# Optimization experiments

Measured on AMD Instinct MI355X. Metric: run time of the kernel, lower is better.

## Reference

```python
import jax, jax.numpy as jnp
import numpy as np

EPS = 1e-8
LN_EPS = 1e-5


def _norm_no_nan(x, axis=-1, keepdims=False):
    return jnp.sqrt(jnp.clip(jnp.sum(x * x, axis=axis, keepdims=keepdims), EPS))


def gvp_apply(s, v, wh, ws_w, ws_b, wv, use_acts):
    # s: [*, si], v: [*, vi, 3]; activations = (relu, sigmoid) when use_acts
    vt = jnp.swapaxes(v, -1, -2)                        # [*, 3, vi]
    vh = jnp.matmul(vt, wh.T)                           # [*, 3, h]
    vn = _norm_no_nan(vh, axis=-2)                      # [*, h]
    s_out = jnp.matmul(jnp.concatenate([s, vn], -1), ws_w.T) + ws_b
    v_out = jnp.swapaxes(jnp.matmul(vh, wv.T), -1, -2)  # [*, vo, 3]
    if use_acts:
        v_out = v_out * jax.nn.sigmoid(_norm_no_nan(v_out, axis=-1, keepdims=True))
        s_out = jax.nn.relu(s_out)
    return s_out, v_out


def tuple_layernorm(s, v, g, b):
    mu = jnp.mean(s, -1, keepdims=True)
    var = jnp.mean(jnp.square(s - mu), -1, keepdims=True)
    s = (s - mu) / jnp.sqrt(var + LN_EPS) * g + b
    vn2 = jnp.clip(jnp.sum(v * v, -1, keepdims=True), EPS)  # [N, nv, 1]
    v = v / jnp.sqrt(jnp.mean(vn2, -2, keepdims=True))
    return s, v


def gvp_conv_layer(node_s, node_v, edge_s, edge_v, edge_index,
                   msg0_wh, msg0_wsw, msg0_wsb, msg0_wv,
                   msg1_wh, msg1_wsw, msg1_wsb, msg1_wv,
                   msg2_wh, msg2_wsw, msg2_wsb, msg2_wv,
                   ln0_g, ln0_b,
                   ff0_wh, ff0_wsw, ff0_wsb, ff0_wv,
                   ff1_wh, ff1_wsw, ff1_wsb, ff1_wv,
                   ln1_g, ln1_b):
    N = node_s.shape[0]
    src, dst = edge_index[0], edge_index[1]  # PyG: x_j = x[edge_index[0]], x_i = x[edge_index[1]]
    # gather + tuple_cat((s_j, v_j), edge_attr, (s_i, v_i))
    ms = jnp.concatenate([node_s[src], edge_s, node_s[dst]], -1)   # [E, 2*ns+es]
    mv = jnp.concatenate([node_v[src], edge_v, node_v[dst]], -2)   # [E, 2*nv+ev, 3]
    # message function: 3 GVPs, last with no activations
    ms, mv = gvp_apply(ms, mv, msg0_wh, msg0_wsw, msg0_wsb, msg0_wv, True)
    ms, mv = gvp_apply(ms, mv, msg1_wh, msg1_wsw, msg1_wsb, msg1_wv, True)
    ms, mv = gvp_apply(ms, mv, msg2_wh, msg2_wsw, msg2_wsb, msg2_wv, False)
    # mean aggregation over incoming edges per target node
    cnt = jax.ops.segment_sum(jnp.ones_like(ms[:, 0]), dst, num_segments=N)
    denom = jnp.maximum(cnt, 1.0)[:, None]
    agg_s = jax.ops.segment_sum(ms, dst, num_segments=N) / denom
    agg_v = jax.ops.segment_sum(mv, dst, num_segments=N) / denom[..., None]
    # residual + LayerNorm (dropout = identity in eval)
    s, v = tuple_layernorm(node_s + agg_s, node_v + agg_v, ln0_g, ln0_b)
    # feedforward: 2 GVPs, hidden (4*ns, 2*nv), last with no activations
    fs, fv = gvp_apply(s, v, ff0_wh, ff0_wsw, ff0_wsb, ff0_wv, True)
    fs, fv = gvp_apply(fs, fv, ff1_wh, ff1_wsw, ff1_wsb, ff1_wv, False)
    return tuple_layernorm(s + fs, v + fv, ln1_g, ln1_b)


def setup_inputs() -> dict:
    key = jax.random.key(0)
    ks = iter(jax.random.split(key, 64))
    N, E = 10000, 200000
    NS, NV, ES, EV = 128, 32, 32, 1

    def _lin(out_d, in_d):
        return jax.random.normal(next(ks), (out_d, in_d), jnp.float32) / np.float32(np.sqrt(in_d))

    inp = {
        'node_s': jax.random.normal(next(ks), (N, NS), jnp.float32),
        'node_v': jax.random.normal(next(ks), (N, NV, 3), jnp.float32),
        'edge_s': jax.random.normal(next(ks), (E, ES), jnp.float32),
        'edge_v': jax.random.normal(next(ks), (E, EV, 3), jnp.float32),
        'edge_index': jax.random.randint(next(ks), (2, E), 0, N, dtype=jnp.int32),
    }
    si0, vi0 = 2 * NS + ES, 2 * NV + EV            # 288, 65
    h0 = max(vi0, NV)                              # 65
    inp['msg0_wh'] = _lin(h0, vi0)
    inp['msg0_wsw'] = _lin(NS, h0 + si0)
    inp['msg0_wsb'] = jnp.zeros((NS,), jnp.float32)
    inp['msg0_wv'] = _lin(NV, h0)
    for name in ('msg1', 'msg2'):
        inp[name + '_wh'] = _lin(NV, NV)
        inp[name + '_wsw'] = _lin(NS, NV + NS)
        inp[name + '_wsb'] = jnp.zeros((NS,), jnp.float32)
        inp[name + '_wv'] = _lin(NV, NV)
    inp['ln0_g'] = jnp.ones((NS,), jnp.float32)
    inp['ln0_b'] = jnp.zeros((NS,), jnp.float32)
    HS, HV = 4 * NS, 2 * NV                        # 512, 64
    hf0 = max(NV, HV)                              # 64
    inp['ff0_wh'] = _lin(hf0, NV)
    inp['ff0_wsw'] = _lin(HS, hf0 + NS)
    inp['ff0_wsb'] = jnp.zeros((HS,), jnp.float32)
    inp['ff0_wv'] = _lin(HV, hf0)
    hf1 = max(HV, NV)                              # 64
    inp['ff1_wh'] = _lin(hf1, HV)
    inp['ff1_wsw'] = _lin(NS, hf1 + HS)
    inp['ff1_wsb'] = jnp.zeros((NS,), jnp.float32)
    inp['ff1_wv'] = _lin(NV, hf1)
    inp['ln1_g'] = jnp.ones((NS,), jnp.float32)
    inp['ln1_b'] = jnp.zeros((NS,), jnp.float32)
    return inp


def reference(node_s, node_v, edge_s, edge_v, edge_index,
              msg0_wh, msg0_wsw, msg0_wsb, msg0_wv,
              msg1_wh, msg1_wsw, msg1_wsb, msg1_wv,
              msg2_wh, msg2_wsw, msg2_wsb, msg2_wv,
              ln0_g, ln0_b,
              ff0_wh, ff0_wsw, ff0_wsb, ff0_wv,
              ff1_wh, ff1_wsw, ff1_wsb, ff1_wv,
              ln1_g, ln1_b):
    return gvp_conv_layer(node_s, node_v, edge_s, edge_v, edge_index,
                          msg0_wh, msg0_wsw, msg0_wsb, msg0_wv,
                          msg1_wh, msg1_wsw, msg1_wsb, msg1_wv,
                          msg2_wh, msg2_wsw, msg2_wsb, msg2_wv,
                          ln0_g, ln0_b,
                          ff0_wh, ff0_wsw, ff0_wsb, ff0_wv,
                          ff1_wh, ff1_wsw, ff1_wsb, ff1_wv,
                          ln1_g, ln1_b)
```

## Files before the change

### kernel.cpp

```cpp
#include <hip/hip_runtime.h>

typedef unsigned short u16;
typedef __attribute__((ext_vector_type(8))) short bf16x8;
typedef __attribute__((ext_vector_type(4))) float f32x4;

__device__ __forceinline__ float b2f(u16 h){ return __uint_as_float(((unsigned)h)<<16); }
__device__ __forceinline__ u16 f2b(float f){
  unsigned u = __float_as_uint(f);
  unsigned r = ((u>>16)&1u) + 0x7fffu;
  return (u16)((u+r)>>16);
}
__device__ __forceinline__ short4 pack4(float4 f){
  short4 s; s.x=(short)f2b(f.x); s.y=(short)f2b(f.y); s.z=(short)f2b(f.z); s.w=(short)f2b(f.w);
  return s;
}

#define WB0   0
#define WB1   49152
#define WB2   69632
#define WBF0  90112
#define WBF1  188416
#define WB_TOTAL 262144

#define V_WH0   0
// ... 86 lines not shown
                                              float* __restrict__ cnt){
  int e = blockIdx.x*256 + threadIdx.x;
  if (e < E) atomicAdd(&cnt[ei[(size_t)E + e]], 1.f);
}

__global__ __launch_bounds__(256) void k_scan(const float* __restrict__ cnt,
                                              int* __restrict__ wpos, int N){
  __shared__ int part[256];
  const int tid = threadIdx.x;
  const int per = (N + 255)/256;
  const int base = tid*per;
  int s = 0;
  for (int i=0;i<per;++i){ int n=base+i; if (n<N) s += (int)cnt[n]; }
  part[tid] = s; __syncthreads();
  for (int st=1; st<256; st<<=1){
    int v = (tid>=st) ? part[tid-st] : 0;
    __syncthreads();
    part[tid] += v;
    __syncthreads();
  }
  int run = part[tid] - s;
  for (int i=0;i<per;++i){ int n=base+i; if (n<N){ wpos[n]=run; run += (int)cnt[n]; } }
}

__global__ __launch_bounds__(256) void k_scatter(const int* __restrict__ ei, int E,
                                                 int* __restrict__ wpos, int* __restrict__ perm){
  int e = blockIdx.x*256 + threadIdx.x;
  if (e >= E) return;
  int d = ei[(size_t)E + e];
  int pos = atomicAdd(&wpos[d], 1);
  perm[pos] = e;
}

#define VEPB 32
__global__ __launch_bounds__(256) void k_edge_v(
    const u16* __restrict__ node_vb, const float* __restrict__ edge_v,
    const int* __restrict__ ei, int E, const int* __restrict__ perm,
    const u16* __restrict__ WVb, u16* __restrict__ vnbuf,
    float* __restrict__ agg_v, int eb, int ec)
{
  __shared__ __align__(16) char UB0[96*104*2];
  __shared__ __align__(16) u16 B1[96][104];
  __shared__ int SD[VEPB][2];
  __shared__ int GE[VEPB];
  u16 (*B0)[104] = (u16(*)[104])UB0;
  float (*SCv)[33] = (float(*)[33])UB0;
  const int tid = threadIdx.x;
  const int w = tid>>6, l = tid&63;
  const int le0 = blockIdx.x*VEPB;

  if (tid < VEPB){
    int le = le0 + tid;
    int ge = (le<ec) ? perm[eb+le] : 0;
    GE[tid] = ge;
    SD[tid][0] = ei[ge];
    SD[tid][1] = ei[(size_t)E + ge];
  }
  __syncthreads();
  for (int u=tid; u<96*16; u+=256){
    int r=u>>4, g=u&15, ee=r/3, d=r-ee*3;
    int le=le0+ee;
    short4 v = {0,0,0,0};
    if (le<ec){
      int node = (g<8) ? SD[ee][0] : SD[ee][1];
      v = *(const short4*)&node_vb[(size_t)node*96 + d*32 + 4*(g&7)];
    }
    *(short4*)&B0[r][4*g] = v;
  }
  for (int u=tid; u<96*8; u+=256){
    int r=u>>3, g=u&7, ee=r/3, d=r-ee*3;
    int le=le0+ee;
    short4 v = {0,0,0,0};
    if (g==0 && le<ec) v.x = (short)f2b(edge_v[(size_t)GE[ee]*3 + d]);
    *(short4*)&B0[r][64+4*g] = v;
  }
  for (int u=tid; u<96*4; u+=256){
    int r=u>>2, g=u&3;
    *(short4*)&B1[r][80+4*g] = (short4){0,0,0,0};
  }
  __syncthreads();

  auto mm = [&](const u16 (*A)[104], int woff, int Kp, int NT, u16 (*C)[104]){
    const int nks = Kp>>5;
    for (int t=w; t<6*NT; t+=4){
      int mt = t % 6, nt = t / 6;
      f32x4 acc = {0.f,0.f,0.f,0.f};
      for (int ks=0; ks<nks; ++ks){
        bf16x8 af = *(const bf16x8*)&A[mt*16 + (l&15)][ks*32 + (l>>4)*8];
        bf16x8 bf = *(const bf16x8*)&WVb[woff + (size_t)(nt*16 + (l&15))*Kp + ks*32 + (l>>4)*8];
        acc = __builtin_amdgcn_mfma_f32_16x16x32_bf16(af, bf, acc, 0, 0, 0);
      }
      const int col = nt*16 + (l&15);
      const int r0 = mt*16 + (l>>4)*4;
      C[r0+0][col]=f2b(acc[0]); C[r0+1][col]=f2b(acc[1]);
      C[r0+2][col]=f2b(acc[2]); C[r0+3][col]=f2b(acc[3]);
    }
  };

  mm(B0, V_WH0, 96, 5, B1);
  __syncthreads();
  for (int u=tid; u<VEPB*80; u+=256){
    int ee=u/80, h=u-ee*80;
    int le=le0+ee;
    if (le<ec){
      u16 val = 0;
      if (h<65){
        float x0=b2f(B1[ee*3+0][h]), x1=b2f(B1[ee*3+1][h]), x2=b2f(B1[ee*3+2][h]);
        val = f2b(sqrtf(fmaxf(x0*x0+x1*x1+x2*x2, 1e-8f)));
      }
      vnbuf[(size_t)le*144 + h] = val;
    }
  }
  mm(B1, V_WV0, 96, 2, B0);
  __syncthreads();
  for (int u=tid; u<VEPB*32; u+=256){
    int ee=u>>5, vo=u&31;
    float x0=b2f(B0[ee*3+0][vo]), x1=b2f(B0[ee*3+1][vo]), x2=b2f(B0[ee*3+2][vo]);
    float nn=sqrtf(fmaxf(x0*x0+x1*x1+x2*x2, 1e-8f));
    float sg=1.f/(1.f+__expf(-nn));
    B0[ee*3+0][vo]=f2b(x0*sg); B0[ee*3+1][vo]=f2b(x1*sg); B0[ee*3+2][vo]=f2b(x2*sg);
  }
  __syncthreads();
  mm(B0, V_WH1, 32, 2, B1);
  __syncthreads();
  for (int u=tid; u<VEPB*32; u+=256){
    int ee=u>>5, h=u&31;
    int le=le0+ee;
    if (le<ec){
      float x0=b2f(B1[ee*3+0][h]), x1=b2f(B1[ee*3+1][h]), x2=b2f(B1[ee*3+2][h]);
      vnbuf[(size_t)le*144 + 80 + h] = f2b(sqrtf(fmaxf(x0*x0+x1*x1+x2*x2, 1e-8f)));
    }
  }
  mm(B1, V_WV1, 32, 2, B0);
  __syncthreads();
  for (int u=tid; u<VEPB*32; u+=256){
    int ee=u>>5, vo=u&31;
    float x0=b2f(B0[ee*3+0][vo]), x1=b2f(B0[ee*3+1][vo]), x2=b2f(B0[ee*3+2][vo]);
    float nn=sqrtf(fmaxf(x0*x0+x1*x1+x2*x2, 1e-8f));
    float sg=1.f/(1.f+__expf(-nn));
    B0[ee*3+0][vo]=f2b(x0*sg); B0[ee*3+1][vo]=f2b(x1*sg); B0[ee*3+2][vo]=f2b(x2*sg);
  }
  __syncthreads();
  mm(B0, V_WH2, 32, 2, B1);
  __syncthreads();
  for (int u=tid; u<VEPB*32; u+=256){
    int ee=u>>5, h=u&31;
    int le=le0+ee;
    if (le<ec){
      float x0=b2f(B1[ee*3+0][h]), x1=b2f(B1[ee*3+1][h]), x2=b2f(B1[ee*3+2][h]);
      vnbuf[(size_t)le*144 + 112 + h] = f2b(sqrtf(fmaxf(x0*x0+x1*x1+x2*x2, 1e-8f)));
    }
  }
  for (int t=w; t<12; t+=4){
    int mt = t % 6, nt = t / 6;
    f32x4 acc = {0.f,0.f,0.f,0.f};
    bf16x8 af = *(const bf16x8*)&B1[mt*16 + (l&15)][(l>>4)*8];
    bf16x8 bf = *(const bf16x8*)&WVb[V_WV2 + (size_t)(nt*16 + (l&15))*32 + (l>>4)*8];
    acc = __builtin_amdgcn_mfma_f32_16x16x32_bf16(af, bf, acc, 0, 0, 0);
    const int vo = nt*16 + (l&15);
    const int r0 = mt*16 + (l>>4)*4;
    #pragma unroll
    for (int j=0;j<4;++j){
      int r = r0 + j;
      int le = le0 + r/3;
      SCv[r][vo] = (le < ec) ? acc[j] : 0.f;
    }
  }
  __syncthreads();
  if (tid < 96){
    const int vo = tid & 31, d = tid >> 5;
    float run = 0.f; int prev = -1;
    for (int ee=0; ee<VEPB; ++ee){
      int le = le0 + ee;
      int dn = (le<ec) ? SD[ee][1] : -1;
      if (dn != prev){
        if (prev >= 0) atomicAdd(&agg_v[(size_t)prev*96 + vo*3 + d], run);
        run = 0.f; prev = dn;
      }
      run += SCv[ee*3+d][vo];
    }
    if (prev >= 0) atomicAdd(&agg_v[(size_t)prev*96 + vo*3 + d], run);
  }
}

#define SPB 32
__global__ __launch_bounds__(512) void k_edge_s(
    const u16* __restrict__ node_sb, const float* __restrict__ edge_s,
    const int* __restrict__ ei, int E, const int* __restrict__ perm,
    const u16* __restrict__ WB, const u16* __restrict__ vnbuf,
    const float* __restrict__ b0p, const float* __restrict__ b1p, const float* __restrict__ b2p,
    float* __restrict__ agg_s, int eb, int ec)
{
  __shared__ __align__(16) char UA[SPB*392*2];
  __shared__ int SD[SPB][2];
  __shared__ int GE[SPB];
  u16 (*A)[392] = (u16(*)[392])UA;
  float (*SC)[132] = (float(*)[132])UA;
  const int tid = threadIdx.x;
  const int le0 = blockIdx.x*SPB;

  if (tid < SPB){
    int le = le0 + tid;
    int ge = (le<ec) ? perm[eb+le] : 0;
    GE[tid] = ge;
    SD[tid][0] = ei[ge];
    SD[tid][1] = ei[(size_t)E + ge];
  }
  __syncthreads();
  for (int u=tid; u<SPB*98; u+=512){
    int ee = u/98, g = u - ee*98;
    int le = le0+ee;
    short4 v = {0,0,0,0};
    if (le<ec){
      if (g < 32)      v = *(const short4*)&node_sb[(size_t)SD[ee][0]*128 + 4*g];
      else if (g < 40) v = pack4(*(const float4*)&edge_s[(size_t)GE[ee]*32 + 4*(g-32)]);
      else if (g < 72) v = *(const short4*)&node_sb[(size_t)SD[ee][1]*128 + 4*(g-40)];
      else if (g < 92) v = *(const short4*)&vnbuf[(size_t)le*144 + 4*(g-72)];
    }
    *(short4*)&A[ee][4*g] = v;
  }
  __syncthreads();

  const int w = tid>>6, l = tid&63;
  const int mt = w>>2, nt = w&3;
  const int n_a = nt*32 + (l&15), n_b = n_a + 16;
  const int kq = (l>>4)*8;
  const int ma = mt*16 + (l&15);
  f32x4 ca = {0.f,0.f,0.f,0.f}, cb = {0.f,0.f,0.f,0.f};

  for (int kk=0; kk<384; kk+=32){
    bf16x8 af = *(const bf16x8*)&A[ma][kk + kq];
    bf16x8 b1 = *(const bf16x8*)&WB[WB0 + (size_t)n_a*384 + kk + kq];
    bf16x8 b2 = *(const bf16x8*)&WB[WB0 + (size_t)n_b*384 + kk + kq];
    ca = __builtin_amdgcn_mfma_f32_16x16x32_bf16(af, b1, ca, 0, 0, 0);
    cb = __builtin_amdgcn_mfma_f32_16x16x32_bf16(af, b2, cb, 0, 0, 0);
  }
  __syncthreads();
  {
    float ba = b0p[n_a], bb = b0p[n_b];
    #pragma unroll
    for (int j=0;j<4;++j){
      int r = mt*16 + (l>>4)*4 + j;
      A[r][n_a] = f2b(fmaxf(ca[j] + ba, 0.f));
      A[r][n_b] = f2b(fmaxf(cb[j] + bb, 0.f));
    }
  }
  for (int u=tid; u<SPB*8; u+=512){
    int ee=u>>3, q=u&7;
    int le=le0+ee;
    short4 v = {0,0,0,0};
    if (le<ec) v = *(const short4*)&vnbuf[(size_t)le*144 + 80 + 4*q];
    *(short4*)&A[ee][128+4*q] = v;
  }
  __syncthreads();

  ca = (f32x4){0.f,0.f,0.f,0.f}; cb = (f32x4){0.f,0.f,0.f,0.f};
  for (int kk=0; kk<160; kk+=32){
    bf16x8 af = *(const bf16x8*)&A[ma][kk + kq];
    bf16x8 b1 = *(const bf16x8*)&WB[WB1 + (size_t)n_a*160 + kk + kq];
    bf16x8 b2 = *(const bf16x8*)&WB[WB1 + (size_t)n_b*160 + kk + kq];
    ca = __builtin_amdgcn_mfma_f32_16x16x32_bf16(af, b1, ca, 0, 0, 0);
    cb = __builtin_amdgcn_mfma_f32_16x16x32_bf16(af, b2, cb, 0, 0, 0);
  }
  __syncthreads();
  {
    float ba = b1p[n_a], bb = b1p[n_b];
    #pragma unroll
    for (int j=0;j<4;++j){
      int r = mt*16 + (l>>4)*4 + j;
      A[r][n_a] = f2b(fmaxf(ca[j] + ba, 0.f));
      A[r][n_b] = f2b(fmaxf(cb[j] + bb, 0.f));
    }
  }
  for (int u=tid; u<SPB*8; u+=512){
    int ee=u>>3, q=u&7;
    int le=le0+ee;
    short4 v = {0,0,0,0};
    if (le<ec) v = *(const short4*)&vnbuf[(size_t)le*144 + 112 + 4*q];
    *(short4*)&A[ee][128+4*q] = v;
  }
  __syncthreads();

  ca = (f32x4){0.f,0.f,0.f,0.f}; cb = (f32x4){0.f,0.f,0.f,0.f};
  for (int kk=0; kk<160; kk+=32){
    bf16x8 af = *(const bf16x8*)&A[ma][kk + kq];
    bf16x8 b1 = *(const bf16x8*)&WB[WB2 + (size_t)n_a*160 + kk + kq];
    bf16x8 b2 = *(const bf16x8*)&WB[WB2 + (size_t)n_b*160 + kk + kq];
    ca = __builtin_amdgcn_mfma_f32_16x16x32_bf16(af, b1, ca, 0, 0, 0);
    cb = __builtin_amdgcn_mfma_f32_16x16x32_bf16(af, b2, cb, 0, 0, 0);
  }
  __syncthreads();
  {
    float ba = b2p[n_a], bb = b2p[n_b];
    #pragma unroll
    for (int j=0;j<4;++j){
      int r = mt*16 + (l>>4)*4 + j;
      int le = le0 + r;
      SC[r][n_a] = (le<ec) ? (ca[j] + ba) : 0.f;
      SC[r][n_b] = (le<ec) ? (cb[j] + bb) : 0.f;
    }
  }
  __syncthreads();
  if (tid < 128){
    const int c = tid;
    float run = 0.f; int prev = -1;
    for (int r=0; r<SPB; ++r){
      int le = le0 + r;
      int dn = (le<ec) ? SD[r][1] : -1;
      if (dn != prev){
        if (prev >= 0) atomicAdd(&agg_s[(size_t)prev*128 + c], run);
        run = 0.f; prev = dn;
      }
      run += SC[r][c];
    }
    if (prev >= 0) atomicAdd(&agg_s[(size_t)prev*128 + c], run);
  }
}

__global__ __launch_bounds__(256) void k_ln0(
    const float* __restrict__ node_s, const float* __restrict__ node_v,
    const float* __restrict__ agg_s, const float* __restrict__ agg_v,
    const float* __restrict__ cnt,
    const float* __restrict__ g, const float* __restrict__ b,
    float* __restrict__ s_mid, float* __restrict__ v_mid, int N)
{
  int n = blockIdx.x*256 + threadIdx.x;
  if (n>=N) return;
  const float inv = 1.f/fmaxf(cnt[n], 1.f);
  float sum=0.f, ss=0.f;
  for (int i=0;i<128;++i){
    float x = node_s[(size_t)n*128+i] + agg_s[(size_t)n*128+i]*inv;
    sum += x; ss += x*x;
  }
  const float mu = sum*(1.f/128.f);
  const float var = fmaxf(ss*(1.f/128.f) - mu*mu, 0.f);
  const float rstd = rsqrtf(var + 1e-5f);
  for (int i=0;i<128;++i){
    float x = node_s[(size_t)n*128+i] + agg_s[(size_t)n*128+i]*inv;
    s_mid[(size_t)n*128+i] = (x-mu)*rstd*g[i] + b[i];
  }
  float vs=0.f;
  for (int vo=0;vo<32;++vo){
    float y0 = node_v[(size_t)n*96+vo*3+0] + agg_v[(size_t)n*96+vo*3+0]*inv;
    float y1 = node_v[(size_t)n*96+vo*3+1] + agg_v[(size_t)n*96+vo*3+1]*inv;
    float y2 = node_v[(size_t)n*96+vo*3+2] + agg_v[(size_t)n*96+vo*3+2]*inv;
    vs += fmaxf(y0*y0+y1*y1+y2*y2, 1e-8f);
  }
  const float scale = rsqrtf(vs*(1.f/32.f));
  for (int vo=0;vo<32;++vo){
    float y0 = node_v[(size_t)n*96+vo*3+0] + agg_v[(size_t)n*96+vo*3+0]*inv;
    float y1 = node_v[(size_t)n*96+vo*3+1] + agg_v[(size_t)n*96+vo*3+1]*inv;
    float y2 = node_v[(size_t)n*96+vo*3+2] + agg_v[(size_t)n*96+vo*3+2]*inv;
    v_mid[(size_t)n*96+vo]      = y0*scale;
    v_mid[(size_t)n*96+32+vo]   = y1*scale;
    v_mid[(size_t)n*96+64+vo]   = y2*scale;
  }
}

__global__ __launch_bounds__(256) void k_node_v(
    const float* __restrict__ v_mid, const u16* __restrict__ WVb,
    u16* __restrict__ vn0f, u16* __restrict__ vn1f, float* __restrict__ fv1, int N)
{
  __shared__ __align__(16) u16 B0[96][104];
  __shared__ __align__(16) u16 B1[96][104];
  const int tid = threadIdx.x;
  const int w = tid>>6, l = tid&63;
  const int n0 = blockIdx.x*32;

  for (int u=tid; u<96*8; u+=256){
    int r=u>>3, g=u&7, nd=r/3, d=r-nd*3;
    int n=n0+nd;
    short4 v = {0,0,0,0};
    if (n<N) v = pack4(*(const float4*)&v_mid[(size_t)n*96 + d*32 + 4*g]);
    *(short4*)&B0[r][4*g] = v;
  }
  __syncthreads();

  auto mm = [&](const u16 (*A)[104], int woff, int Kp, int NT, u16 (*C)[104]){
    const int nks = Kp>>5;
    for (int t=w; t<6*NT; t+=4){
      int mt = t % 6, nt = t / 6;
      f32x4 acc = {0.f,0.f,0.f,0.f};
      for (int ks=0; ks<nks; ++ks){
        bf16x8 af = *(const bf16x8*)&A[mt*16 + (l&15)][ks*32 + (l>>4)*8];
        bf16x8 bf = *(const bf16x8*)&WVb[woff + (size_t)(nt*16 + (l&15))*Kp + ks*32 + (l>>4)*8];
        acc = __builtin_amdgcn_mfma_f32_16x16x32_bf16(af, bf, acc, 0, 0, 0);
      }
      const int col = nt*16 + (l&15);
      const int r0 = mt*16 + (l>>4)*4;
      C[r0+0][col]=f2b(acc[0]); C[r0+1][col]=f2b(acc[1]);
      C[r0+2][col]=f2b(acc[2]); C[r0+3][col]=f2b(acc[3]);
    }
  };

  mm(B0, NV_FF0H, 32, 4, B1);
  __syncthreads();
  for (int u=tid; u<32*64; u+=256){
    int nd=u>>6, h=u&63;
    int n=n0+nd;
    if (n<N){
      float x0=b2f(B1[nd*3+0][h]), x1=b2f(B1[nd*3+1][h]), x2=b2f(B1[nd*3+2][h]);
      vn0f[(size_t)n*64+h] = f2b(sqrtf(fmaxf(x0*x0+x1*x1+x2*x2, 1e-8f)));
    }
  }
  mm(B1, NV_FF0V, 64, 4, B0);
  __syncthreads();
  for (int u=tid; u<32*64; u+=256){
    int nd=u>>6, vo=u&63;
    float x0=b2f(B0[nd*3+0][vo]), x1=b2f(B0[nd*3+1][vo]), x2=b2f(B0[nd*3+2][vo]);
    float nn=sqrtf(fmaxf(x0*x0+x1*x1+x2*x2, 1e-8f));
    float sg=1.f/(1.f+__expf(-nn));
    B0[nd*3+0][vo]=f2b(x0*sg); B0[nd*3+1][vo]=f2b(x1*sg); B0[nd*3+2][vo]=f2b(x2*sg);
  }
  __syncthreads();
  mm(B0, NV_FF1H, 64, 4, B1);
  __syncthreads();
  for (int u=tid; u<32*64; u+=256){
    int nd=u>>6, h=u&63;
    int n=n0+nd;
    if (n<N){
      float x0=b2f(B1[nd*3+0][h]), x1=b2f(B1[nd*3+1][h]), x2=b2f(B1[nd*3+2][h]);
      vn1f[(size_t)n*64+h] = f2b(sqrtf(fmaxf(x0*x0+x1*x1+x2*x2, 1e-8f)));
    }
  }
  for (int t=w; t<12; t+=4){
    int mt = t % 6, nt = t / 6;
    f32x4 acc = {0.f,0.f,0.f,0.f};
// ... 110 lines not shown
      }
    }
    float z[2][3]; float vs = 0.f;
    #pragma unroll
    for (int j=0;j<2;++j){
      int vo = q + 16*j;
      #pragma unroll
      for (int d=0;d<3;++d){
        float y = live ? (v_mid[(size_t)n*96 + d*32 + vo] + fv1[(size_t)n*96 + d*32 + vo]) : 0.f;
        z[j][d] = y;
      }
      vs += fmaxf(z[j][0]*z[j][0]+z[j][1]*z[j][1]+z[j][2]*z[j][2], 1e-8f);
    }
    #pragma unroll
    for (int m=1; m<16; m<<=1) vs += __shfl_xor(vs, m);
    const float scale = rsqrtf(vs*(1.f/32.f));
    if (live){
      size_t base = (size_t)N*128 + (size_t)n*96;
      #pragma unroll
      for (int j=0;j<2;++j){
        int vo = q + 16*j;
        out[base + vo*3 + 0] = z[j][0]*scale;
        out[base + vo*3 + 1] = z[j][1]*scale;
        out[base + vo*3 + 2] = z[j][2]*scale;
      }
    }
  }
}

extern "C" void kernel_launch(void* const* d_in, const int* in_sizes, int n_in,
                              void* d_out, int out_size, void* d_ws, size_t ws_size,
                              hipStream_t stream)
{
  (void)n_in; (void)out_size;
  const int N = in_sizes[0]/128;
  const int E = in_sizes[4]/2;
  const int* ei = (const int*)d_in[4];

  size_t off = 0;
  auto alloc = [&](size_t bytes)->char*{
    size_t o = (off + 255) & ~(size_t)255;
    off = o + bytes;
    return (char*)d_ws + o;
  };
  u16*   WB      = (u16*)alloc((size_t)WB_TOTAL*2);
  u16*   WVb     = (u16*)alloc((size_t)WV_TOTAL*2);
  float* agg_s   = (float*)alloc((size_t)N*128*4);
  float* agg_v   = (float*)alloc((size_t)N*96*4);
  float* cnt     = (float*)alloc((size_t)N*4);
  size_t aggBytes = (size_t)((char*)(cnt+N) - (char*)agg_s);
  float* s_mid   = (float*)alloc((size_t)N*128*4);
  float* v_mid   = (float*)alloc((size_t)N*96*4);
  u16*   node_sb = (u16*)alloc((size_t)N*128*2);
  u16*   node_vb = (u16*)alloc((size_t)N*96*2);
  u16*   vn0f    = (u16*)alloc((size_t)N*64*2);
  u16*   vn1f    = (u16*)alloc((size_t)N*64*2);
  float* fv1     = (float*)alloc((size_t)N*96*4);
  int*   wpos    = (int*)alloc((size_t)N*4);
  int*   perm    = (int*)alloc((size_t)E*4);
  const size_t persist_end = off;

  size_t avail = (ws_size > persist_end + (1u<<20)) ? (ws_size - persist_end - (1u<<20)) : 0;
  long EC = (long)(avail / 288);
  if (EC < 8192) EC = 8192;
  if (EC > E) EC = E;
  u16* vnbuf = (u16*)alloc((size_t)EC*144*2);

  hipMemsetAsync(agg_s, 0, aggBytes, stream);
  k_wb<<<dim3((WB_TOTAL+255)/256), dim3(256), 0, stream>>>(
      (const float*)d_in[6], (const float*)d_in[10], (const float*)d_in[14],
      (const float*)d_in[20], (const float*)d_in[24], WB);
  k_wv<<<dim3((WV_TOTAL+255)/256), dim3(256), 0, stream>>>(
      (const float*)d_in[5], (const float*)d_in[8], (const float*)d_in[9],
      (const float*)d_in[12], (const float*)d_in[13], (const float*)d_in[16],
      (const float*)d_in[19], (const float*)d_in[22], (const float*)d_in[23],
      (const float*)d_in[26], WVb);
  k_prep<<<dim3((N*224+255)/256), dim3(256), 0, stream>>>(
      (const float*)d_in[0], (const float*)d_in[1], node_sb, node_vb, N);
  k_hist<<<dim3((E+255)/256), dim3(256), 0, stream>>>(ei, E, cnt);
  k_scan<<<dim3(1), dim3(256), 0, stream>>>(cnt, wpos, N);
  k_scatter<<<dim3((E+255)/256), dim3(256), 0, stream>>>(ei, E, wpos, perm);

  const int nch = (int)((E + EC - 1)/EC);
  for (int c=0; c<nch; ++c){
    const int eb = c*(int)EC;
    int ec = E - eb; if (ec > (int)EC) ec = (int)EC;
    if (ec <= 0) break;
    k_edge_v<<<dim3((ec+VEPB-1)/VEPB), dim3(256), 0, stream>>>(
        node_vb, (const float*)d_in[3], ei, E, perm, WVb, vnbuf, agg_v, eb, ec);
    k_edge_s<<<dim3((ec+SPB-1)/SPB), dim3(512), 0, stream>>>(
        node_sb, (const float*)d_in[2], ei, E, perm, WB, vnbuf,
        (const float*)d_in[7], (const float*)d_in[11], (const float*)d_in[15],
        agg_s, eb, ec);
  }

  k_ln0<<<dim3((N+255)/256), dim3(256), 0, stream>>>(
      (const float*)d_in[0], (const float*)d_in[1], agg_s, agg_v, cnt,
      (const float*)d_in[17], (const float*)d_in[18], s_mid, v_mid, N);

  k_node_v<<<dim3((N+31)/32), dim3(256), 0, stream>>>(v_mid, WVb, vn0f, vn1f, fv1, N);
  k_node_s<<<dim3((N+31)/32), dim3(512), 0, stream>>>(
      s_mid, vn0f, vn1f, v_mid, fv1, WB,
      (const float*)d_in[21], (const float*)d_in[25],
      (const float*)d_in[27], (const float*)d_in[28],
      (float*)d_out, N);
}
```

Measured before the change: 587.4 us.

## Fuse edge vector and scalar message kernels into one block-level kernel

Merges the separate edge-vector and edge-scalar kernels into a single 512-thread kernel, so the vector-norm features stay in shared memory instead of making a round trip through a global vnbuf. The chunked edge loop and its workspace sizing go away, and the whole edge set is launched at once. The vector-GVP matmuls now spread their tiles over 8 waves instead of 4, and the kernel's shared-memory footprint grows to about 50KB, which may reduce occupancy.

Measured after the change: 568.6 us. 3.2% less time.

```diff
diff --git a/kernel.cpp b/kernel.cpp
--- a/kernel.cpp
+++ b/kernel.cpp
@@ -142,51 +142,315 @@
   perm[pos] = e;
 }
 
-#define VEPB 32
-__global__ __launch_bounds__(256) void k_edge_v(
-    const u16* __restrict__ node_vb, const float* __restrict__ edge_v,
+#define EPB 32
+__global__ __launch_bounds__(512) void k_edge_fused(
+    const u16* __restrict__ node_sb, const u16* __restrict__ node_vb,
+    const float* __restrict__ edge_s, const float* __restrict__ edge_v,
     const int* __restrict__ ei, int E, const int* __restrict__ perm,
-    const u16* __restrict__ WVb, u16* __restrict__ vnbuf,
-    float* __restrict__ agg_v, int eb, int ec)
+    const u16* __restrict__ WB, const u16* __restrict__ WVb,
+    const float* __restrict__ b0p, const float* __restrict__ b1p, const float* __restrict__ b2p,
+    float* __restrict__ agg_s, float* __restrict__ agg_v)
 {
-  __shared__ __align__(16) char UB0[96*104*2];
-  __shared__ __align__(16) u16 B1[96][104];
-  __shared__ int SD[VEPB][2];
-  __shared__ int GE[VEPB];
-  u16 (*B0)[104] = (u16(*)[104])UB0;
-  float (*SCv)[33] = (float(*)[33])UB0;
+  __shared__ __align__(16) char R1[42240];
+  __shared__ __align__(16) u16 VN0[EPB][80];
+  __shared__ __align__(16) u16 VN1[EPB][32];
+  __shared__ __align__(16) u16 VN2[EPB][32];
+  __shared__ int SD[EPB][2];
+  __shared__ int GE[EPB];
+  u16 (*B0)[104]  = (u16(*)[104])R1;
+  u16 (*B1)[104]  = (u16(*)[104])(R1 + 20480);
+  float (*SCv)[33] = (float(*)[33])R1;
+  u16 (*A)[392]   = (u16(*)[392])R1;
+  float (*SC)[132] = (float(*)[132])R1;
+
   const int tid = threadIdx.x;
   const int w = tid>>6, l = tid&63;
-  const int le0 = blockIdx.x*VEPB;
-
-  if (tid < VEPB){
+  const int le0 = blockIdx.x*EPB;
+
+  if (tid < EPB){
     int le = le0 + tid;
-    int ge = (le<ec) ? perm[eb+le] : 0;
+    int ge = (le<E) ? perm[le] : 0;
     GE[tid] = ge;
     SD[tid][0] = ei[ge];
     SD[tid][1] = ei[(size_t)E + ge];
   }
   __syncthreads();
-  for (int u=tid; u<96*16; u+=256){
+  for (int u=tid; u<96*16; u+=512){
     int r=u>>4, g=u&15, ee=r/3, d=r-ee*3;
     int le=le0+ee;
     short4 v = {0,0,0,0};
-    if (le<ec){
+    if (le<E){
       int node = (g<8) ? SD[ee][0] : SD[ee][1];
       v = *(const short4*)&node_vb[(size_t)node*96 + d*32 + 4*(g&7)];
     }
     *(short4*)&B0[r][4*g] = v;
   }
-  for (int u=tid; u<96*8; u+=256){
+  for (int u=tid; u<96*8; u+=512){
     int r=u>>3, g=u&7, ee=r/3, d=r-ee*3;
     int le=le0+ee;
     short4 v = {0,0,0,0};
-    if (g==0 && le<ec) v.x = (short)f2b(edge_v[(size_t)GE[ee]*3 + d]);
+    if (g==0 && le<E) v.x = (short)f2b(edge_v[(size_t)GE[ee]*3 + d]);
     *(short4*)&B0[r][64+4*g] = v;
   }
-  for (int u=tid; u<96*4; u+=256){
+  for (int u=tid; u<96*4; u+=512){
     int r=u>>2, g=u&3;
     *(short4*)&B1[r][80+4*g] = (short4){0,0,0,0};
+  }
+  __syncthreads();
+
+  auto mm = [&](const u16 (*Ai)[104], int woff, int Kp, int NT, u16 (*C)[104]){
+    const int nks = Kp>>5;
+    for (int t=w; t<6*NT; t+=8){
+      int mt = t % 6, nt = t / 6;
+      f32x4 acc = {0.f,0.f,0.f,0.f};
+      for (int ks=0; ks<nks; ++ks){
+        bf16x8 af = *(const bf16x8*)&Ai[mt*16 + (l&15)][ks*32 + (l>>4)*8];
+        bf16x8 bf = *(const bf16x8*)&WVb[woff + (size_t)(nt*16 + (l&15))*Kp + ks*32 + (l>>4)*8];
+        acc = __builtin_amdgcn_mfma_f32_16x16x32_bf16(af, bf, acc, 0, 0, 0);
+      }
+      const int col = nt*16 + (l&15);
+      const int r0 = mt*16 + (l>>4)*4;
+      C[r0+0][col]=f2b(acc[0]); C[r0+1][col]=f2b(acc[1]);
+      C[r0+2][col]=f2b(acc[2]); C[r0+3][col]=f2b(acc[3]);
+    }
+  };
+
+  mm(B0, V_WH0, 96, 5, B1);
+  __syncthreads();
+  for (int u=tid; u<EPB*80; u+=512){
+    int ee=u/80, h=u-ee*80;
+    u16 val = 0;
+    if (h<65){
+      float x0=b2f(B1[ee*3+0][h]), x1=b2f(B1[ee*3+1][h]), x2=b2f(B1[ee*3+2][h]);
+      val = f2b(sqrtf(fmaxf(x0*x0+x1*x1+x2*x2, 1e-8f)));
+    }
+    VN0[ee][h] = val;
+  }
+  mm(B1, V_WV0, 96, 2, B0);
+  __syncthreads();
+  for (int u=tid; u<EPB*32; u+=512){
+    int ee=u>>5, vo=u&31;
+    float x0=b2f(B0[ee*3+0][vo]), x1=b2f(B0[ee*3+1][vo]), x2=b2f(B0[ee*3+2][vo]);
+    float nn=sqrtf(fmaxf(x0*x0+x1*x1+x2*x2, 1e-8f));
+    float sg=1.f/(1.f+__expf(-nn));
+    B0[ee*3+0][vo]=f2b(x0*sg); B0[ee*3+1][vo]=f2b(x1*sg); B0[ee*3+2][vo]=f2b(x2*sg);
+  }
+  __syncthreads();
+  mm(B0, V_WH1, 32, 2, B1);
+  __syncthreads();
+  for (int u=tid; u<EPB*32; u+=512){
+    int ee=u>>5, h=u&31;
+    float x0=b2f(B1[ee*3+0][h]), x1=b2f(B1[ee*3+1][h]), x2=b2f(B1[ee*3+2][h]);
+    VN1[ee][h] = f2b(sqrtf(fmaxf(x0*x0+x1*x1+x2*x2, 1e-8f)));
+  }
+  mm(B1, V_WV1, 32, 2, B0);
+  __syncthreads();
+  for (int u=tid; u<EPB*32; u+=512){
+    int ee=u>>5, vo=u&31;
+    float x0=b2f(B0[ee*3+0][vo]), x1=b2f(B0[ee*3+1][vo]), x2=b2f(B0[ee*3+2][vo]);
+    float nn=sqrtf(fmaxf(x0*x0+x1*x1+x2*x2, 1e-8f));
+    float sg=1.f/(1.f+__expf(-nn));
+    B0[ee*3+0][vo]=f2b(x0*sg); B0[ee*3+1][vo]=f2b(x1*sg); B0[ee*3+2][vo]=f2b(x2*sg);
+  }
+  __syncthreads();
+  mm(B0, V_WH2, 32, 2, B1);
+  __syncthreads();
+  for (int u=tid; u<EPB*32; u+=512){
+    int ee=u>>5, h=u&31;
+    float x0=b2f(B1[ee*3+0][h]), x1=b2f(B1[ee*3+1][h]), x2=b2f(B1[ee*3+2][h]);
+    VN2[ee][h] = f2b(sqrtf(fmaxf(x0*x0+x1*x1+x2*x2, 1e-8f)));
+  }
+  for (int t=w; t<12; t+=8){
+    int mt = t % 6, nt = t / 6;
+    f32x4 acc = {0.f,0.f,0.f,0.f};
+    bf16x8 af = *(const bf16x8*)&B1[mt*16 + (l&15)][(l>>4)*8];
+    bf16x8 bf = *(const bf16x8*)&WVb[V_WV2 + (size_t)(nt*16 + (l&15))*32 + (l>>4)*8];
+    acc = __builtin_amdgcn_mfma_f32_16x16x32_bf16(af, bf, acc, 0, 0, 0);
+    const int vo = nt*16 + (l&15);
+    const int r0 = mt*16 + (l>>4)*4;
+    #pragma unroll
+    for (int j=0;j<4;++j){
+      int r = r0 + j;
+      int le = le0 + r/3;
+      SCv[r][vo] = (le < E) ? acc[j] : 0.f;
+    }
+  }
+  __syncthreads();
+  if (tid < 96){
+    const int vo = tid & 31, d = tid >> 5;
+    float run = 0.f; int prev = -1;
+    for (int ee=0; ee<EPB; ++ee){
+      int le = le0 + ee;
+      int dn = (le<E) ? SD[ee][1] : -1;
+      if (dn != prev){
+        if (prev >= 0) atomicAdd(&agg_v[(size_t)prev*96 + vo*3 + d], run);
+        run = 0.f; prev = dn;
+      }
+      run += SCv[ee*3+d][vo];
+    }
+    if (prev >= 0) atomicAdd(&agg_v[(size_t)prev*96 + vo*3 + d], run);
+  }
+  __syncthreads();
+
+  for (int u=tid; u<EPB*98; u+=512){
+    int ee = u/98, g = u - ee*98;
+    int le = le0+ee;
+    short4 v = {0,0,0,0};
+    if (le<E){
+      if (g < 32)      v = *(const short4*)&node_sb[(size_t)SD[ee][0]*128 + 4*g];
+      else if (g < 40) v = pack4(*(const float4*)&edge_s[(size_t)GE[ee]*32 + 4*(g-32)]);
+      else if (g < 72) v = *(const short4*)&node_sb[(size_t)SD[ee][1]*128 + 4*(g-40)];
+      else if (g < 92) v = *(const short4*)&VN0[ee][4*(g-72)];
+    }
+    *(short4*)&A[ee][4*g] = v;
+  }
+  __syncthreads();
+
+  const int mt = w>>2, nt = w&3;
+  const int n_a = nt*32 + (l&15), n_b = n_a + 16;
+  const int kq = (l>>4)*8;
+  const int ma = mt*16 + (l&15);
+  f32x4 ca = {0.f,0.f,0.f,0.f}, cb = {0.f,0.f,0.f,0.f};
+
+  for (int kk=0; kk<384; kk+=32){
+    bf16x8 af = *(const bf16x8*)&A[ma][kk + kq];
+    bf16x8 b1 = *(const bf16x8*)&WB[WB0 + (size_t)n_a*384 + kk + kq];
+    bf16x8 b2 = *(const bf16x8*)&WB[WB0 + (size_t)n_b*384 + kk + kq];
+    ca = __builtin_amdgcn_mfma_f32_16x16x32_bf16(af, b1, ca, 0, 0, 0);
+    cb = __builtin_amdgcn_mfma_f32_16x16x32_bf16(af, b2, cb, 0, 0, 0);
+  }
+  __syncthreads();
+  {
+    float ba = b0p[n_a], bb = b0p[n_b];
+    #pragma unroll
+    for (int j=0;j<4;++j){
+      int r = mt*16 + (l>>4)*4 + j;
+      A[r][n_a] = f2b(fmaxf(ca[j] + ba, 0.f));
+      A[r][n_b] = f2b(fmaxf(cb[j] + bb, 0.f));
+    }
+  }
+  for (int u=tid; u<EPB*8; u+=512){
+    int ee=u>>3, q=u&7;
+    *(short4*)&A[ee][128+4*q] = *(const short4*)&VN1[ee][4*q];
+  }
+  __syncthreads();
+
+  ca = (f32x4){0.f,0.f,0.f,0.f}; cb = (f32x4){0.f,0.f,0.f,0.f};
+  for (int kk=0; kk<160; kk+=32){
+    bf16x8 af = *(const bf16x8*)&A[ma][kk + kq];
+    bf16x8 b1 = *(const bf16x8*)&WB[WB1 + (size_t)n_a*160 + kk + kq];
+    bf16x8 b2 = *(const bf16x8*)&WB[WB1 + (size_t)n_b*160 + kk + kq];
+    ca = __builtin_amdgcn_mfma_f32_16x16x32_bf16(af, b1, ca, 0, 0, 0);
+    cb = __builtin_amdgcn_mfma_f32_16x16x32_bf16(af, b2, cb, 0, 0, 0);
+  }
+  __syncthreads();
+  {
+    float ba = b1p[n_a], bb = b1p[n_b];
+    #pragma unroll
+    for (int j=0;j<4;++j){
+      int r = mt*16 + (l>>4)*4 + j;
+      A[r][n_a] = f2b(fmaxf(ca[j] + ba, 0.f));
+      A[r][n_b] = f2b(fmaxf(cb[j] + bb, 0.f));
+    }
+  }
+  for (int u=tid; u<EPB*8; u+=512){
+    int ee=u>>3, q=u&7;
+    *(short4*)&A[ee][128+4*q] = *(const short4*)&VN2[ee][4*q];
+  }
+  __syncthreads();
+
+  ca = (f32x4){0.f,0.f,0.f,0.f}; cb = (f32x4){0.f,0.f,0.f,0.f};
+  for (int kk=0; kk<160; kk+=32){
+    bf16x8 af = *(const bf16x8*)&A[ma][kk + kq];
+    bf16x8 b1 = *(const bf16x8*)&WB[WB2 + (size_t)n_a*160 + kk + kq];
+    bf16x8 b2 = *(const bf16x8*)&WB[WB2 + (size_t)n_b*160 + kk + kq];
+    ca = __builtin_amdgcn_mfma_f32_16x16x32_bf16(af, b1, ca, 0, 0, 0);
+    cb = __builtin_amdgcn_mfma_f32_16x16x32_bf16(af, b2, cb, 0, 0, 0);
+  }
+  __syncthreads();
+  {
+    float ba = b2p[n_a], bb = b2p[n_b];
+    #pragma unroll
+    for (int j=0;j<4;++j){
+      int r = mt*16 + (l>>4)*4 + j;
+      int le = le0 + r;
+      SC[r][n_a] = (le<E) ? (ca[j] + ba) : 0.f;
+      SC[r][n_b] = (le<E) ? (cb[j] + bb) : 0.f;
+    }
+  }
+  __syncthreads();
+  if (tid < 128){
+    const int c = tid;
+    float run = 0.f; int prev = -1;
+    for (int r=0; r<EPB; ++r){
+      int le = le0 + r;
+      int dn = (le<E) ? SD[r][1] : -1;
+      if (dn != prev){
+        if (prev >= 0) atomicAdd(&agg_s[(size_t)prev*128 + c], run);
+        run = 0.f; prev = dn;
+      }
+      run += SC[r][c];
+    }
+    if (prev >= 0) atomicAdd(&agg_s[(size_t)prev*128 + c], run);
+  }
+}
+
+__global__ __launch_bounds__(256) void k_ln0(
+    const float* __restrict__ node_s, const float* __restrict__ node_v,
+    const float* __restrict__ agg_s, const float* __restrict__ agg_v,
+    const float* __restrict__ cnt,
+    const float* __restrict__ g, const float* __restrict__ b,
+    float* __restrict__ s_mid, float* __restrict__ v_mid, int N)
+{
+  int n = blockIdx.x*256 + threadIdx.x;
+  if (n>=N) return;
+  const float inv = 1.f/fmaxf(cnt[n], 1.f);
+  float sum=0.f, ss=0.f;
+  for (int i=0;i<128;++i){
+    float x = node_s[(size_t)n*128+i] + agg_s[(size_t)n*128+i]*inv;
+    sum += x; ss += x*x;
+  }
+  const float mu = sum*(1.f/128.f);
+  const float var = fmaxf(ss*(1.f/128.f) - mu*mu, 0.f);
+  const float rstd = rsqrtf(var + 1e-5f);
+  for (int i=0;i<128;++i){
+    float x = node_s[(size_t)n*128+i] + agg_s[(size_t)n*128+i]*inv;
+    s_mid[(size_t)n*128+i] = (x-mu)*rstd*g[i] + b[i];
+  }
+  float vs=0.f;
+  for (int vo=0;vo<32;++vo){
+    float y0 = node_v[(size_t)n*96+vo*3+0] + agg_v[(size_t)n*96+vo*3+0]*inv;
+    float y1 = node_v[(size_t)n*96+vo*3+1] + agg_v[(size_t)n*96+vo*3+1]*inv;
+    float y2 = node_v[(size_t)n*96+vo*3+2] + agg_v[(size_t)n*96+vo*3+2]*inv;
+    vs += fmaxf(y0*y0+y1*y1+y2*y2, 1e-8f);
+  }
+  const float scale = rsqrtf(vs*(1.f/32.f));
+  for (int vo=0;vo<32;++vo){
+    float y0 = node_v[(size_t)n*96+vo*3+0] + agg_v[(size_t)n*96+vo*3+0]*inv;
+    float y1 = node_v[(size_t)n*96+vo*3+1] + agg_v[(size_t)n*96+vo*3+1]*inv;
+    float y2 = node_v[(size_t)n*96+vo*3+2] + agg_v[(size_t)n*96+vo*3+2]*inv;
+    v_mid[(size_t)n*96+vo]      = y0*scale;
+    v_mid[(size_t)n*96+32+vo]   = y1*scale;
+    v_mid[(size_t)n*96+64+vo]   = y2*scale;
+  }
+}
+
+__global__ __launch_bounds__(256) void k_node_v(
+    const float* __restrict__ v_mid, const u16* __restrict__ WVb,
+    u16* __restrict__ vn0f, u16* __restrict__ vn1f, float* __restrict__ fv1, int N)
+{
+  __shared__ __align__(16) u16 B0[96][104];
+  __shared__ __align__(16) u16 B1[96][104];
+  const int tid = threadIdx.x;
+  const int w = tid>>6, l = tid&63;
+  const int n0 = blockIdx.x*32;
+
+  for (int u=tid; u<96*8; u+=256){
+    int r=u>>3, g=u&7, nd=r/3, d=r-nd*3;
+    int n=n0+nd;
+    short4 v = {0,0,0,0};
+    if (n<N) v = pack4(*(const float4*)&v_mid[(size_t)n*96 + d*32 + 4*g]);
+    *(short4*)&B0[r][4*g] = v;
   }
   __syncthreads();
 
@@ -207,302 +471,6 @@
     }
   };
 
-  mm(B0, V_WH0, 96, 5, B1);
-  __syncthreads();
-  for (int u=tid; u<VEPB*80; u+=256){
-    int ee=u/80, h=u-ee*80;
-    int le=le0+ee;
-    if (le<ec){
-      u16 val = 0;
-      if (h<65){
-        float x0=b2f(B1[ee*3+0][h]), x1=b2f(B1[ee*3+1][h]), x2=b2f(B1[ee*3+2][h]);
-        val = f2b(sqrtf(fmaxf(x0*x0+x1*x1+x2*x2, 1e-8f)));
-      }
-      vnbuf[(size_t)le*144 + h] = val;
-    }
-  }
-  mm(B1, V_WV0, 96, 2, B0);
-  __syncthreads();
-  for (int u=tid; u<VEPB*32; u+=256){
-    int ee=u>>5, vo=u&31;
-    float x0=b2f(B0[ee*3+0][vo]), x1=b2f(B0[ee*3+1][vo]), x2=b2f(B0[ee*3+2][vo]);
-    float nn=sqrtf(fmaxf(x0*x0+x1*x1+x2*x2, 1e-8f));
-    float sg=1.f/(1.f+__expf(-nn));
-    B0[ee*3+0][vo]=f2b(x0*sg); B0[ee*3+1][vo]=f2b(x1*sg); B0[ee*3+2][vo]=f2b(x2*sg);
-  }
-  __syncthreads();
-  mm(B0, V_WH1, 32, 2, B1);
-  __syncthreads();
-  for (int u=tid; u<VEPB*32; u+=256){
-    int ee=u>>5, h=u&31;
-    int le=le0+ee;
-    if (le<ec){
-      float x0=b2f(B1[ee*3+0][h]), x1=b2f(B1[ee*3+1][h]), x2=b2f(B1[ee*3+2][h]);
-      vnbuf[(size_t)le*144 + 80 + h] = f2b(sqrtf(fmaxf(x0*x0+x1*x1+x2*x2, 1e-8f)));
-    }
-  }
-  mm(B1, V_WV1, 32, 2, B0);
-  __syncthreads();
-  for (int u=tid; u<VEPB*32; u+=256){
-    int ee=u>>5, vo=u&31;
-    float x0=b2f(B0[ee*3+0][vo]), x1=b2f(B0[ee*3+1][vo]), x2=b2f(B0[ee*3+2][vo]);
-    float nn=sqrtf(fmaxf(x0*x0+x1*x1+x2*x2, 1e-8f));
-    float sg=1.f/(1.f+__expf(-nn));
-    B0[ee*3+0][vo]=f2b(x0*sg); B0[ee*3+1][vo]=f2b(x1*sg); B0[ee*3+2][vo]=f2b(x2*sg);
-  }
-  __syncthreads();
-  mm(B0, V_WH2, 32, 2, B1);
-  __syncthreads();
-  for (int u=tid; u<VEPB*32; u+=256){
-    int ee=u>>5, h=u&31;
-    int le=le0+ee;
-    if (le<ec){
-      float x0=b2f(B1[ee*3+0][h]), x1=b2f(B1[ee*3+1][h]), x2=b2f(B1[ee*3+2][h]);
-      vnbuf[(size_t)le*144 + 112 + h] = f2b(sqrtf(fmaxf(x0*x0+x1*x1+x2*x2, 1e-8f)));
-    }
-  }
-  for (int t=w; t<12; t+=4){
-    int mt = t % 6, nt = t / 6;
-    f32x4 acc = {0.f,0.f,0.f,0.f};
-    bf16x8 af = *(const bf16x8*)&B1[mt*16 + (l&15)][(l>>4)*8];
-    bf16x8 bf = *(const bf16x8*)&WVb[V_WV2 + (size_t)(nt*16 + (l&15))*32 + (l>>4)*8];
-    acc = __builtin_amdgcn_mfma_f32_16x16x32_bf16(af, bf, acc, 0, 0, 0);
-    const int vo = nt*16 + (l&15);
-    const int r0 = mt*16 + (l>>4)*4;
-    #pragma unroll
-    for (int j=0;j<4;++j){
-      int r = r0 + j;
-      int le = le0 + r/3;
-      SCv[r][vo] = (le < ec) ? acc[j] : 0.f;
-    }
-  }
-  __syncthreads();
-  if (tid < 96){
-    const int vo = tid & 31, d = tid >> 5;
-    float run = 0.f; int prev = -1;
-    for (int ee=0; ee<VEPB; ++ee){
-      int le = le0 + ee;
-      int dn = (le<ec) ? SD[ee][1] : -1;
-      if (dn != prev){
-        if (prev >= 0) atomicAdd(&agg_v[(size_t)prev*96 + vo*3 + d], run);
-        run = 0.f; prev = dn;
-      }
-      run += SCv[ee*3+d][vo];
-    }
-    if (prev >= 0) atomicAdd(&agg_v[(size_t)prev*96 + vo*3 + d], run);
-  }
-}
-
-#define SPB 32
-__global__ __launch_bounds__(512) void k_edge_s(
-    const u16* __restrict__ node_sb, const float* __restrict__ edge_s,
-    const int* __restrict__ ei, int E, const int* __restrict__ perm,
-    const u16* __restrict__ WB, const u16* __restrict__ vnbuf,
-    const float* __restrict__ b0p, const float* __restrict__ b1p, const float* __restrict__ b2p,
-    float* __restrict__ agg_s, int eb, int ec)
-{
-  __shared__ __align__(16) char UA[SPB*392*2];
-  __shared__ int SD[SPB][2];
-  __shared__ int GE[SPB];
-  u16 (*A)[392] = (u16(*)[392])UA;
-  float (*SC)[132] = (float(*)[132])UA;
-  const int tid = threadIdx.x;
-  const int le0 = blockIdx.x*SPB;
-
-  if (tid < SPB){
-    int le = le0 + tid;
-    int ge = (le<ec) ? perm[eb+le] : 0;
-    GE[tid] = ge;
-    SD[tid][0] = ei[ge];
-    SD[tid][1] = ei[(size_t)E + ge];
-  }
-  __syncthreads();
-  for (int u=tid; u<SPB*98; u+=512){
-    int ee = u/98, g = u - ee*98;
-    int le = le0+ee;
-    short4 v = {0,0,0,0};
-    if (le<ec){
-      if (g < 32)      v = *(const short4*)&node_sb[(size_t)SD[ee][0]*128 + 4*g];
-      else if (g < 40) v = pack4(*(const float4*)&edge_s[(size_t)GE[ee]*32 + 4*(g-32)]);
-      else if (g < 72) v = *(const short4*)&node_sb[(size_t)SD[ee][1]*128 + 4*(g-40)];
-      else if (g < 92) v = *(const short4*)&vnbuf[(size_t)le*144 + 4*(g-72)];
-    }
-    *(short4*)&A[ee][4*g] = v;
-  }
-  __syncthreads();
-
-  const int w = tid>>6, l = tid&63;
-  const int mt = w>>2, nt = w&3;
-  const int n_a = nt*32 + (l&15), n_b = n_a + 16;
-  const int kq = (l>>4)*8;
-  const int ma = mt*16 + (l&15);
-  f32x4 ca = {0.f,0.f,0.f,0.f}, cb = {0.f,0.f,0.f,0.f};
-
-  for (int kk=0; kk<384; kk+=32){
-    bf16x8 af = *(const bf16x8*)&A[ma][kk + kq];
-    bf16x8 b1 = *(const bf16x8*)&WB[WB0 + (size_t)n_a*384 + kk + kq];
-    bf16x8 b2 = *(const bf16x8*)&WB[WB0 + (size_t)n_b*384 + kk + kq];
-    ca = __builtin_amdgcn_mfma_f32_16x16x32_bf16(af, b1, ca, 0, 0, 0);
-    cb = __builtin_amdgcn_mfma_f32_16x16x32_bf16(af, b2, cb, 0, 0, 0);
-  }
-  __syncthreads();
-  {
-    float ba = b0p[n_a], bb = b0p[n_b];
-    #pragma unroll
-    for (int j=0;j<4;++j){
-      int r = mt*16 + (l>>4)*4 + j;
-      A[r][n_a] = f2b(fmaxf(ca[j] + ba, 0.f));
-      A[r][n_b] = f2b(fmaxf(cb[j] + bb, 0.f));
-    }
-  }
-  for (int u=tid; u<SPB*8; u+=512){
-    int ee=u>>3, q=u&7;
-    int le=le0+ee;
-    short4 v = {0,0,0,0};
-    if (le<ec) v = *(const short4*)&vnbuf[(size_t)le*144 + 80 + 4*q];
-    *(short4*)&A[ee][128+4*q] = v;
-  }
-  __syncthreads();
-
-  ca = (f32x4){0.f,0.f,0.f,0.f}; cb = (f32x4){0.f,0.f,0.f,0.f};
-  for (int kk=0; kk<160; kk+=32){
-    bf16x8 af = *(const bf16x8*)&A[ma][kk + kq];
-    bf16x8 b1 = *(const bf16x8*)&WB[WB1 + (size_t)n_a*160 + kk + kq];
-    bf16x8 b2 = *(const bf16x8*)&WB[WB1 + (size_t)n_b*160 + kk + kq];
-    ca = __builtin_amdgcn_mfma_f32_16x16x32_bf16(af, b1, ca, 0, 0, 0);
-    cb = __builtin_amdgcn_mfma_f32_16x16x32_bf16(af, b2, cb, 0, 0, 0);
-  }
-  __syncthreads();
-  {
-    float ba = b1p[n_a], bb = b1p[n_b];
-    #pragma unroll
-    for (int j=0;j<4;++j){
-      int r = mt*16 + (l>>4)*4 + j;
-      A[r][n_a] = f2b(fmaxf(ca[j] + ba, 0.f));
-      A[r][n_b] = f2b(fmaxf(cb[j] + bb, 0.f));
-    }
-  }
-  for (int u=tid; u<SPB*8; u+=512){
-    int ee=u>>3, q=u&7;
-    int le=le0+ee;
-    short4 v = {0,0,0,0};
-    if (le<ec) v = *(const short4*)&vnbuf[(size_t)le*144 + 112 + 4*q];
-    *(short4*)&A[ee][128+4*q] = v;
-  }
-  __syncthreads();
-
-  ca = (f32x4){0.f,0.f,0.f,0.f}; cb = (f32x4){0.f,0.f,0.f,0.f};
-  for (int kk=0; kk<160; kk+=32){
-    bf16x8 af = *(const bf16x8*)&A[ma][kk + kq];
-    bf16x8 b1 = *(const bf16x8*)&WB[WB2 + (size_t)n_a*160 + kk + kq];
-    bf16x8 b2 = *(const bf16x8*)&WB[WB2 + (size_t)n_b*160 + kk + kq];
-    ca = __builtin_amdgcn_mfma_f32_16x16x32_bf16(af, b1, ca, 0, 0, 0);
-    cb = __builtin_amdgcn_mfma_f32_16x16x32_bf16(af, b2, cb, 0, 0, 0);
-  }
-  __syncthreads();
-  {
-    float ba = b2p[n_a], bb = b2p[n_b];
-    #pragma unroll
-    for (int j=0;j<4;++j){
-      int r = mt*16 + (l>>4)*4 + j;
-      int le = le0 + r;
-      SC[r][n_a] = (le<ec) ? (ca[j] + ba) : 0.f;
-      SC[r][n_b] = (le<ec) ? (cb[j] + bb) : 0.f;
-    }
-  }
-  __syncthreads();
-  if (tid < 128){
-    const int c = tid;
-    float run = 0.f; int prev = -1;
-    for (int r=0; r<SPB; ++r){
-      int le = le0 + r;
-      int dn = (le<ec) ? SD[r][1] : -1;
-      if (dn != prev){
-        if (prev >= 0) atomicAdd(&agg_s[(size_t)prev*128 + c], run);
-        run = 0.f; prev = dn;
-      }
-      run += SC[r][c];
-    }
-    if (prev >= 0) atomicAdd(&agg_s[(size_t)prev*128 + c], run);
-  }
-}
-
-__global__ __launch_bounds__(256) void k_ln0(
-    const float* __restrict__ node_s, const float* __restrict__ node_v,
-    const float* __restrict__ agg_s, const float* __restrict__ agg_v,
-    const float* __restrict__ cnt,
-    const float* __restrict__ g, const float* __restrict__ b,
-    float* __restrict__ s_mid, float* __restrict__ v_mid, int N)
-{
-  int n = blockIdx.x*256 + threadIdx.x;
-  if (n>=N) return;
-  const float inv = 1.f/fmaxf(cnt[n], 1.f);
-  float sum=0.f, ss=0.f;
-  for (int i=0;i<128;++i){
-    float x = node_s[(size_t)n*128+i] + agg_s[(size_t)n*128+i]*inv;
-    sum += x; ss += x*x;
-  }
-  const float mu = sum*(1.f/128.f);
-  const float var = fmaxf(ss*(1.f/128.f) - mu*mu, 0.f);
-  const float rstd = rsqrtf(var + 1e-5f);
-  for (int i=0;i<128;++i){
-    float x = node_s[(size_t)n*128+i] + agg_s[(size_t)n*128+i]*inv;
-    s_mid[(size_t)n*128+i] = (x-mu)*rstd*g[i] + b[i];
-  }
-  float vs=0.f;
-  for (int vo=0;vo<32;++vo){
-    float y0 = node_v[(size_t)n*96+vo*3+0] + agg_v[(size_t)n*96+vo*3+0]*inv;
-    float y1 = node_v[(size_t)n*96+vo*3+1] + agg_v[(size_t)n*96+vo*3+1]*inv;
-    float y2 = node_v[(size_t)n*96+vo*3+2] + agg_v[(size_t)n*96+vo*3+2]*inv;
-    vs += fmaxf(y0*y0+y1*y1+y2*y2, 1e-8f);
-  }
-  const float scale = rsqrtf(vs*(1.f/32.f));
-  for (int vo=0;vo<32;++vo){
-    float y0 = node_v[(size_t)n*96+vo*3+0] + agg_v[(size_t)n*96+vo*3+0]*inv;
-    float y1 = node_v[(size_t)n*96+vo*3+1] + agg_v[(size_t)n*96+vo*3+1]*inv;
-    float y2 = node_v[(size_t)n*96+vo*3+2] + agg_v[(size_t)n*96+vo*3+2]*inv;
-    v_mid[(size_t)n*96+vo]      = y0*scale;
-    v_mid[(size_t)n*96+32+vo]   = y1*scale;
-    v_mid[(size_t)n*96+64+vo]   = y2*scale;
-  }
-}
-
-__global__ __launch_bounds__(256) void k_node_v(
-    const float* __restrict__ v_mid, const u16* __restrict__ WVb,
-    u16* __restrict__ vn0f, u16* __restrict__ vn1f, float* __restrict__ fv1, int N)
-{
-  __shared__ __align__(16) u16 B0[96][104];
-  __shared__ __align__(16) u16 B1[96][104];
-  const int tid = threadIdx.x;
-  const int w = tid>>6, l = tid&63;
-  const int n0 = blockIdx.x*32;
-
-  for (int u=tid; u<96*8; u+=256){
-    int r=u>>3, g=u&7, nd=r/3, d=r-nd*3;
-    int n=n0+nd;
-    short4 v = {0,0,0,0};
-    if (n<N) v = pack4(*(const float4*)&v_mid[(size_t)n*96 + d*32 + 4*g]);
-    *(short4*)&B0[r][4*g] = v;
-  }
-  __syncthreads();
-
-  auto mm = [&](const u16 (*A)[104], int woff, int Kp, int NT, u16 (*C)[104]){
-    const int nks = Kp>>5;
-    for (int t=w; t<6*NT; t+=4){
-      int mt = t % 6, nt = t / 6;
-      f32x4 acc = {0.f,0.f,0.f,0.f};
-      for (int ks=0; ks<nks; ++ks){
-        bf16x8 af = *(const bf16x8*)&A[mt*16 + (l&15)][ks*32 + (l>>4)*8];
-        bf16x8 bf = *(const bf16x8*)&WVb[woff + (size_t)(nt*16 + (l&15))*Kp + ks*32 + (l>>4)*8];
-        acc = __builtin_amdgcn_mfma_f32_16x16x32_bf16(af, bf, acc, 0, 0, 0);
-      }
-      const int col = nt*16 + (l&15);
-      const int r0 = mt*16 + (l>>4)*4;
-      C[r0+0][col]=f2b(acc[0]); C[r0+1][col]=f2b(acc[1]);
-      C[r0+2][col]=f2b(acc[2]); C[r0+3][col]=f2b(acc[3]);
-    }
-  };
-
   mm(B0, NV_FF0H, 32, 4, B1);
   __syncthreads();
   for (int u=tid; u<32*64; u+=256){
@@ -679,7 +647,7 @@
                               void* d_out, int out_size, void* d_ws, size_t ws_size,
                               hipStream_t stream)
 {
-  (void)n_in; (void)out_size;
+  (void)n_in; (void)out_size; (void)ws_size;
   const int N = in_sizes[0]/128;
   const int E = in_sizes[4]/2;
   const int* ei = (const int*)d_in[4];
@@ -705,13 +673,6 @@
   float* fv1     = (float*)alloc((size_t)N*96*4);
   int*   wpos    = (int*)alloc((size_t)N*4);
   int*   perm    = (int*)alloc((size_t)E*4);
-  const size_t persist_end = off;
-
-  size_t avail = (ws_size > persist_end + (1u<<20)) ? (ws_size - persist_end - (1u<<20)) : 0;
-  long EC = (long)(avail / 288);
-  if (EC < 8192) EC = 8192;
-  if (EC > E) EC = E;
-  u16* vnbuf = (u16*)alloc((size_t)EC*144*2);
 
   hipMemsetAsync(agg_s, 0, aggBytes, stream);
   k_wb<<<dim3((WB_TOTAL+255)/256), dim3(256), 0, stream>>>(
@@ -728,18 +689,11 @@
   k_scan<<<dim3(1), dim3(256), 0, stream>>>(cnt, wpos, N);
   k_scatter<<<dim3((E+255)/256), dim3(256), 0, stream>>>(ei, E, wpos, perm);
 
-  const int nch = (int)((E + EC - 1)/EC);
-  for (int c=0; c<nch; ++c){
-    const int eb = c*(int)EC;
-    int ec = E - eb; if (ec > (int)EC) ec = (int)EC;
-    if (ec <= 0) break;
-    k_edge_v<<<dim3((ec+VEPB-1)/VEPB), dim3(256), 0, stream>>>(
-        node_vb, (const float*)d_in[3], ei, E, perm, WVb, vnbuf, agg_v, eb, ec);
-    k_edge_s<<<dim3((ec+SPB-1)/SPB), dim3(512), 0, stream>>>(
-        node_sb, (const float*)d_in[2], ei, E, perm, WB, vnbuf,
-        (const float*)d_in[7], (const float*)d_in[11], (const float*)d_in[15],
-        agg_s, eb, ec);
-  }
+  k_edge_fused<<<dim3((E+EPB-1)/EPB), dim3(512), 0, stream>>>(
+      node_sb, node_vb, (const float*)d_in[2], (const float*)d_in[3],
+      ei, E, perm, WB, WVb,
+      (const float*)d_in[7], (const float*)d_in[11], (const float*)d_in[15],
+      agg_s, agg_v);
 
   k_ln0<<<dim3((N+255)/256), dim3(256), 0, stream>>>(
       (const float*)d_in[0], (const float*)d_in[1], agg_s, agg_v, cnt,
```
